# Kernel tuning notes

Hardware: AMD Instinct MI355X
Metric: run time of the kernel (lower is better)

The kernel has to match this reference:

```python
import jax, jax.numpy as jnp
import numpy as np

# static config matching init_kwargs
NODE, K, KER, STR = 32, 10, 5, 2
B, C = 8, 64
N = NODE * NODE          # 1024 nodes per sample
BN = B * N               # 8192 total nodes
OUT = (NODE - KER) // STR + 1
E = OUT * OUT            # local hyperedges per sample (196)
BN_EPS = 1e-5


def _local_block_diag():
    """Static block-diagonal local incidence matrix (BN, B*E), built once in numpy."""
    idx = np.arange(N).reshape(NODE, NODE)
    H_local = np.zeros((N, E), np.float32)
    e = 0
    for i in range(0, NODE - KER + 1, STR):
        for j in range(0, NODE - KER + 1, STR):
            H_local[idx[i:i + KER, j:j + KER].ravel(), e] = 1.0
            e += 1
    blk = np.zeros((BN, B * E), np.float32)
    for b in range(B):
        blk[b * N:(b + 1) * N, b * E:(b + 1) * E] = H_local
    return jnp.asarray(blk)


_LOCAL_BLK = _local_block_diag()


def setup_inputs() -> dict:
    key = jax.random.key(0)
    k1, k2 = jax.random.split(key, 2)
    x = jax.random.normal(k1, (B, N, C), jnp.float32)
    W_conv = jax.random.normal(k2, (C, C), jnp.float32) * 0.05
    b_conv = jnp.zeros((C,), jnp.float32)
    gamma = jnp.ones((C,), jnp.float32)
    beta = jnp.zeros((C,), jnp.float32)
    return {"x": x, "W_conv": W_conv, "b_conv": b_conv, "gamma": gamma, "beta": beta}


def reference(x, W_conv, b_conv, gamma, beta):
    xm = x.reshape(BN, C)                       # merged nodes (B*N, C)

    # --- hypergraph construction (no_grad in torch) ---
    xs = jax.lax.stop_gradient(xm)
    sq = jnp.sum(xs * xs, axis=-1, keepdims=True)
    dists = sq - 2.0 * (xs @ xs.T) + sq.T       # (BN, BN) pairwise sq-dists
    _, inds = jax.lax.top_k(-dists, K + 1)      # K+1 smallest distances
    # weights_function(prob=False) -> all ones; scatter incidence
    H = jnp.zeros((BN, BN), x.dtype).at[jnp.arange(BN)[:, None], inds].set(1.0)
    # Dv == K+1 for every row -> max_k = K+1 and the second topk gives new_H == H
    Hfull = jnp.concatenate([H, _LOCAL_BLK], axis=1)  # (BN, BN + B*E)

    # G = Dv^{-1/2} H W De^{-1} H^T Dv^{-1/2}, W = I, via diagonal scaling
    DV = Hfull.sum(axis=1)
    DE = jnp.maximum(Hfull.sum(axis=0), 1e-8)
    dv2 = DV ** -0.5
    A = dv2[:, None] * Hfull
    G = (A * (1.0 / DE)[None, :]) @ A.T          # (BN, BN)
    G = jax.lax.stop_gradient(G)

    # --- HGNN conv: linear -> G matmul -> BN (train stats) -> relu -> residual ---
    y = xm @ W_conv.T + b_conv                   # (BN, C)
    z = G @ y                                    # (BN, C)
    mu = z.mean(axis=0)
    var = z.var(axis=0)                          # biased, as torch BN training
    zn = (z - mu) / jnp.sqrt(var + BN_EPS) * gamma + beta
    out = jax.nn.relu(zn) + xm
    return out.reshape(B, N, C)
```

## Files before the change

kernel.cpp:

```cpp
#include <hip/hip_runtime.h>
#include <math.h>

#define BNTOT 8192
#define CH    64
#define KP1   11
#define NLOC  1568
#define CAP   256
#define LCAP  32
#define MARGIN 1.0f
#define DELTA  2.0f

typedef __attribute__((ext_vector_type(8))) short short8;
typedef __attribute__((ext_vector_type(4))) float float4v;

__device__ __forceinline__ int pcnt(int p) {
  int lo = p - 4; if (lo < 0) lo = 0; lo += (lo & 1);
  int hi = p; if (hi > 26) hi = 26;
  return (hi >= lo) ? (((hi - lo) >> 1) + 1) : 0;
}
__device__ __forceinline__ float dv2_of(int u) {
  int node = u & 1023;
  int rr = node >> 5, cc = node & 31;
  int dv = KP1 + pcnt(rr) * pcnt(cc);
  return 1.0f / sqrtf((float)dv);
}
__device__ __forceinline__ unsigned short f2bf(float f) {
  unsigned u = __float_as_uint(f);
  unsigned r = (u + 0x7FFFu + ((u >> 16) & 1u)) >> 16;
  return (unsigned short)r;
}
__device__ __forceinline__ unsigned long long skey(float s, int idx) {
  unsigned u = __float_as_uint(s);
  u = (u & 0x80000000u) ? ~u : (u | 0x80000000u);
  return ((unsigned long long)u << 32) | (unsigned)idx;
}

__global__ void k_cast(const float* __restrict__ X, unsigned short* __restrict__ Xh,
                       float* __restrict__ sq) {
  int g = blockIdx.x * 256 + threadIdx.x;
  int lane = threadIdx.x & 63;
  float v = X[g];
  Xh[g] = f2bf(v);
  float s = v * v;
  #pragma unroll
  for (int off = 32; off >= 1; off >>= 1) s += __shfl_xor(s, off, 64);
  if (lane == 0) sq[g >> 6] = s;
}

__global__ __launch_bounds__(256)
void k_thrpart(const float* __restrict__ X, const float* __restrict__ sq,
               float* __restrict__ part) {
  const int tid = threadIdx.x, wave = tid >> 6, lane = tid & 63;
  const int rg = blockIdx.x >> 3, chunk = blockIdx.x & 7;
  const int row = rg * 64 + lane;
  float xr[CH];
  {
    const float4* xp = (const float4*)(X + (size_t)row * CH);
    #pragma unroll
    for (int k = 0; k < CH / 4; ++k) {
      float4 v = xp[k];
      xr[4*k+0] = v.x; xr[4*k+1] = v.y; xr[4*k+2] = v.z; xr[4*k+3] = v.w;
    }
  }
  float tv[KP1];
  #pragma unroll
  for (int t = 0; t < KP1; ++t) tv[t] = INFINITY;

  for (int s = 0; s < 32; ++s) {
    int j = __builtin_amdgcn_readfirstlane(((chunk * 4 + wave) * 32 + s) * 8);
    const float* cp = X + (size_t)j * CH;
    float d0 = 0.f, d1 = 0.f, d2 = 0.f, d3 = 0.f;
    #pragma unroll
    for (int k = 0; k < CH / 4; ++k) {
      d0 = fmaf(xr[4*k+0], cp[4*k+0], d0);
      d1 = fmaf(xr[4*k+1], cp[4*k+1], d1);
      d2 = fmaf(xr[4*k+2], cp[4*k+2], d2);
      d3 = fmaf(xr[4*k+3], cp[4*k+3], d3);
    }
    float cv = fmaf(-2.0f, (d0 + d1) + (d2 + d3), sq[j]);
    #pragma unroll
    for (int t = 0; t < KP1; ++t) {
      float lo = fminf(tv[t], cv), hi = fmaxf(tv[t], cv);
      tv[t] = lo; cv = hi;
    }
  }
  __shared__ float ls[4][64][KP1];
  #pragma unroll
  for (int t = 0; t < KP1; ++t) ls[wave][lane][t] = tv[t];
  __syncthreads();
  if (tid < 64) {
    float v[KP1];
    #pragma unroll
    for (int t = 0; t < KP1; ++t) v[t] = ls[0][tid][t];
    #pragma unroll
    for (int w = 1; w < 4; ++w)
      #pragma unroll
      for (int t = 0; t < KP1; ++t) {
        float cv = ls[w][tid][t];
        #pragma unroll
        for (int s2 = 0; s2 < KP1; ++s2) {
          float lo = fminf(v[s2], cv), hi = fmaxf(v[s2], cv);
          v[s2] = lo; cv = hi;
        }
      }
    size_t base = ((size_t)blockIdx.x * 64 + tid) * KP1;
    #pragma unroll
    for (int t = 0; t < KP1; ++t) part[base + t] = v[t];
  }
}

__global__ void k_thrmerge(const float* __restrict__ part, float* __restrict__ thr) {
  const int rg = blockIdx.x, lane = threadIdx.x;
  const int row = rg * 64 + lane;
  float v[KP1];
  {
    size_t b0 = ((size_t)(rg * 8) * 64 + lane) * KP1;
    #pragma unroll
    for (int t = 0; t < KP1; ++t) v[t] = part[b0 + t];
  }
  for (int c = 1; c < 8; ++c) {
    size_t b = ((size_t)(rg * 8 + c) * 64 + lane) * KP1;
    #pragma unroll
    for (int t = 0; t < KP1; ++t) {
      float cv = part[b + t];
      #pragma unroll
      for (int s2 = 0; s2 < KP1; ++s2) {
        float lo = fminf(v[s2], cv), hi = fmaxf(v[s2], cv);
        v[s2] = lo; cv = hi;
      }
    }
  }
  thr[row] = v[KP1 - 1] + MARGIN;
}

__global__ __launch_bounds__(256)
void k_filter(const unsigned short* __restrict__ Xh, const float* __restrict__ sq,
              const float* __restrict__ thr, int* __restrict__ cnt,
              uint2* __restrict__ cand) {
  __shared__ uint2 lcand[64][LCAP];
  __shared__ int lcnt[64];
  __shared__ int lbase[64];

  const int tid = threadIdx.x, wave = tid >> 6, lane = tid & 63;
  const int m = lane & 15, q = lane >> 4;
  const int rowbase = (blockIdx.x >> 5) * 64;
  const int colbase = (blockIdx.x & 31) * 256 + wave * 64;

  if (tid < 64) lcnt[tid] = 0;

  short8 a[4][2];
  #pragma unroll
  for (int rt = 0; rt < 4; ++rt)
    #pragma unroll
    for (int kc = 0; kc < 2; ++kc)
      a[rt][kc] = *(const short8*)(Xh + (size_t)(rowbase + rt * 16 + m) * CH + kc * 32 + q * 8);

  short8 b0[4], b1[4];
  float sqv[4];
  #pragma unroll
  for (int sub = 0; sub < 4; ++sub) {
    const int coln = colbase + sub * 16 + m;
    const short8* bp = (const short8*)(Xh + (size_t)coln * CH + q * 8);
    b0[sub] = bp[0];
    b1[sub] = bp[4];
    sqv[sub] = sq[coln];
  }

  float thrv[16];
  #pragma unroll
  for (int rt = 0; rt < 4; ++rt)
    #pragma unroll
    for (int r = 0; r < 4; ++r)
      thrv[rt * 4 + r] = thr[rowbase + rt * 16 + q * 4 + r];

  __syncthreads();

  const float4v cz = {0.f, 0.f, 0.f, 0.f};
  #pragma unroll
  for (int sub = 0; sub < 4; ++sub) {
    const int coln = colbase + sub * 16 + m;
    #pragma unroll
    for (int rt = 0; rt < 4; ++rt) {
      float4v c = __builtin_amdgcn_mfma_f32_16x16x32_bf16(a[rt][0], b0[sub], cz, 0, 0, 0);
      c = __builtin_amdgcn_mfma_f32_16x16x32_bf16(a[rt][1], b1[sub], c, 0, 0, 0);
      #pragma unroll
      for (int r = 0; r < 4; ++r) {
        float score = fmaf(-2.0f, c[r], sqv[sub]);
        if (score < thrv[rt * 4 + r]) {
          int rl = rt * 16 + q * 4 + r;
          uint2 ent; ent.x = (unsigned)coln; ent.y = __float_as_uint(score);
          int s = atomicAdd(&lcnt[rl], 1);
          if (s < LCAP) {
            lcand[rl][s] = ent;
          } else {
            int gs = atomicAdd(&cnt[rowbase + rl], 1);
            if (gs < CAP) cand[(size_t)(rowbase + rl) * CAP + gs] = ent;
          }
        }
      }
    }
  }

  __syncthreads();
  if (tid < 64) {
    int nl = lcnt[tid]; if (nl > LCAP) nl = LCAP;
    lbase[tid] = atomicAdd(&cnt[rowbase + tid], nl);
    lcnt[tid] = nl;
  }
  __syncthreads();
  if (tid < 64) {
    int nl = lcnt[tid], base = lbase[tid];
    uint2* dst = cand + (size_t)(rowbase + tid) * CAP;
    for (int s = 0; s < nl; ++s) {
      int g = base + s;
      if (g < CAP) dst[g] = lcand[tid][s];
    }
  }
}

__global__ __launch_bounds__(256)
void k_rescore(const float* __restrict__ X, const float* __restrict__ sq,
               const int* __restrict__ cnt, const uint2* __restrict__ cand,
               int* __restrict__ inds, int* __restrict__ DE) {
  const int tid = threadIdx.x, lane = tid & 63;
  const int row = __builtin_amdgcn_readfirstlane(blockIdx.x * 4 + (tid >> 6));

  float xr[CH];
  {
    const float4* xp = (const float4*)(X + (size_t)row * CH);
    #pragma unroll
    for (int k = 0; k < CH / 4; ++k) {
      float4 v = xp[k];
      xr[4*k+0] = v.x; xr[4*k+1] = v.y; xr[4*k+2] = v.z; xr[4*k+3] = v.w;
    }
  }
  const int nraw = cnt[row];

  float tv[KP1]; int ti[KP1];
  #pragma unroll
  for (int t = 0; t < KP1; ++t) { tv[t] = INFINITY; ti[t] = -1; }

  if (nraw <= CAP) {
    const int n = nraw;
    const int slotcnt = (n + 63) >> 6;

    float bsc[4]; int bcol[4];
    #pragma unroll
    for (int a = 0; a < 4; ++a) { bsc[a] = INFINITY; bcol[a] = -1; }
    for (int a = 0; a < slotcnt; ++a) {
      int s = a * 64 + lane;
      if (s < n) {
        uint2 e = cand[(size_t)row * CAP + s];
        bcol[a] = (int)e.x; bsc[a] = __uint_as_float(e.y);
      }
    }
    float curf = bsc[0];
    #pragma unroll
    for (int a = 1; a < 4; ++a) curf = fminf(curf, bsc[a]);
    float c11 = INFINITY;
    #pragma unroll
    for (int t = 0; t < KP1; ++t) {
      float mw = curf;
      #pragma unroll
      for (int off = 1; off < 64; off <<= 1) mw = fminf(mw, __shfl_xor(mw, off, 64));
      if (t == KP1 - 1) c11 = mw;
      if (curf == mw) curf = INFINITY;
    }
    const float cutoff = c11 + DELTA;

    for (int a = 0; a < slotcnt; ++a) {
      if (bsc[a] <= cutoff) {
        int cj = bcol[a];
        const float4* cp = (const float4*)(X + (size_t)cj * CH);
        float d0 = 0.f, d1 = 0.f, d2 = 0.f, d3 = 0.f;
        #pragma unroll
        for (int k = 0; k < CH / 4; ++k) {
          float4 v = cp[k];
          d0 = fmaf(xr[4*k+0], v.x, d0);
          d1 = fmaf(xr[4*k+1], v.y, d1);
          d2 = fmaf(xr[4*k+2], v.z, d2);
          d3 = fmaf(xr[4*k+3], v.w, d3);
        }
        float score = fmaf(-2.0f, (d0 + d1) + (d2 + d3), sq[cj]);
        if (score < tv[KP1 - 1]) {
          float cv = score; int ci = cj;
          #pragma unroll
          for (int t = 0; t < KP1; ++t) {
            bool sw = cv < tv[t];
            float nv = sw ? cv   : tv[t]; int ni = sw ? ci   : ti[t];
            float ov = sw ? tv[t] : cv;   int oi = sw ? ti[t] : ci;
            tv[t] = nv; ti[t] = ni; cv = ov; ci = oi;
          }
        }
      }
    }
  } else {
    for (int s = lane; s < BNTOT; s += 64) {
      const float4* cp = (const float4*)(X + (size_t)s * CH);
      float d0 = 0.f, d1 = 0.f, d2 = 0.f, d3 = 0.f;
      #pragma unroll
      for (int k = 0; k < CH / 4; ++k) {
        float4 v = cp[k];
        d0 = fmaf(xr[4*k+0], v.x, d0);
        d1 = fmaf(xr[4*k+1], v.y, d1);
        d2 = fmaf(xr[4*k+2], v.z, d2);
        d3 = fmaf(xr[4*k+3], v.w, d3);
      }
      float score = fmaf(-2.0f, (d0 + d1) + (d2 + d3), sq[s]);
      if (score < tv[KP1 - 1]) {
        float cv = score; int ci = s;
        #pragma unroll
        for (int t = 0; t < KP1; ++t) {
          bool sw = cv < tv[t];
          float nv = sw ? cv   : tv[t]; int ni = sw ? ci   : ti[t];
          float ov = sw ? tv[t] : cv;   int oi = sw ? ti[t] : ci;
          tv[t] = nv; ti[t] = ni; cv = ov; ci = oi;
        }
      }
    }
  }

  unsigned long long cur = skey(tv[0], ti[0]);
  unsigned long long keep = 0;
  #pragma unroll
  for (int t = 0; t < KP1; ++t) {
    unsigned long long mw = cur;
    #pragma unroll
    for (int off = 1; off < 64; off <<= 1) {
      unsigned lo = __shfl_xor((unsigned)mw, off, 64);
      unsigned hi = __shfl_xor((unsigned)(mw >> 32), off, 64);
      unsigned long long o = ((unsigned long long)hi << 32) | lo;
      mw = (o < mw) ? o : mw;
    }
    if (lane == t) keep = mw;
    if (cur == mw) {
      #pragma unroll
      for (int q = 0; q < KP1 - 1; ++q) { tv[q] = tv[q+1]; ti[q] = ti[q+1]; }
      tv[KP1-1] = INFINITY; ti[KP1-1] = -1;
      cur = skey(tv[0], ti[0]);
    }
  }
  if (lane < KP1) {
    int idx = (int)(unsigned)(keep & 0xFFFFFFFFull);
    inds[(size_t)row * KP1 + lane] = idx;
    atomicAdd(&DE[idx], 1);
  }
}

__global__ void k_lin(const float* __restrict__ X, const float* __restrict__ W,
                      const float* __restrict__ bias, float* __restrict__ t) {
  int lane = threadIdx.x & 63;
  int wave = threadIdx.x >> 6;
  int rowbase = (blockIdx.x * 4 + wave) * 4;
  float wr[CH];
  {
    const float4* wp = (const float4*)(W + (size_t)lane * CH);
    #pragma unroll
    for (int k = 0; k < CH / 4; ++k) {
      float4 v = wp[k];
      wr[4*k+0] = v.x; wr[4*k+1] = v.y; wr[4*k+2] = v.z; wr[4*k+3] = v.w;
    }
  }
  float bc = bias[lane];
  #pragma unroll
  for (int r = 0; r < 4; ++r) {
    int row = __builtin_amdgcn_readfirstlane(rowbase + r);
    const float* xp = X + (size_t)row * CH;
    float d0 = 0.f, d1 = 0.f, d2 = 0.f, d3 = 0.f;
    #pragma unroll
    for (int k = 0; k < CH / 4; ++k) {
      d0 = fmaf(wr[4*k+0], xp[4*k+0], d0);
      d1 = fmaf(wr[4*k+1], xp[4*k+1], d1);
      d2 = fmaf(wr[4*k+2], xp[4*k+2], d2);
      d3 = fmaf(wr[4*k+3], xp[4*k+3], d3);
    }
    float y = (d0 + d1) + (d2 + d3) + bc;
    t[(size_t)row * CH + lane] = y * dv2_of(row);
  }
}

__global__ void k_edge(const float* __restrict__ t, const int* __restrict__ inds,
                       float* __restrict__ s_knn, float* __restrict__ s_loc) {
  int c = threadIdx.x & 63;
  int w = threadIdx.x >> 6;
  if (blockIdx.x < BNTOT / 4) {
    int u = blockIdx.x * 4 + w;
    float val = t[(size_t)u * CH + c];
    int ub = __builtin_amdgcn_readfirstlane(u);
    const int* ip = inds + (size_t)ub * KP1;
    #pragma unroll
    for (int j = 0; j < KP1; ++j) {
      int e = ip[j];
      atomicAdd(&s_knn[(size_t)e * CH + c], val);
    }
  } else {
    int e = (blockIdx.x - BNTOT / 4) * 4 + w;
    int b  = e / 196;
    int le = e - b * 196;
    int pi = le / 14;
    int pj = le - pi * 14;
    int base = b * 1024 + (pi * 2) * 32 + pj * 2;
    float acc = 0.f;
    #pragma unroll
    for (int di = 0; di < 5; ++di)
      #pragma unroll
      for (int dj = 0; dj < 5; ++dj)
        acc += t[(size_t)(base + di * 32 + dj) * CH + c];
    s_loc[(size_t)e * CH + c] = acc * (1.0f / 25.0f);
  }
}

__global__ void k_gatherbn(const float* __restrict__ s_knn, const float* __restrict__ s_loc,
                           const int* __restrict__ inds, const int* __restrict__ DE,
                           float* __restrict__ z, float* __restrict__ part,
                           float* __restrict__ partsq) {
  int c = threadIdx.x & 63;
  int w = threadIdx.x >> 6;
  int u = blockIdx.x * 4 + w;
  int ub = __builtin_amdgcn_readfirstlane(u);
  const int* ip = inds + (size_t)ub * KP1;
  float acc = 0.f;
  #pragma unroll
  for (int j = 0; j < KP1; ++j) {
    int e = ip[j];
    float invde = 1.0f / (float)DE[e];
    acc += s_knn[(size_t)e * CH + c] * invde;
  }
  int node = ub & 1023, b = ub >> 10;
  int rr = node >> 5, cc = node & 31;
  int i0 = rr - 4; if (i0 < 0) i0 = 0; i0 += (i0 & 1);
  int i1 = rr; if (i1 > 26) i1 = 26;
  int j0 = cc - 4; if (j0 < 0) j0 = 0; j0 += (j0 & 1);
  int j1 = cc; if (j1 > 26) j1 = 26;
  for (int i = i0; i <= i1; i += 2)
    for (int jj = j0; jj <= j1; jj += 2) {
      int e = b * 196 + (i >> 1) * 14 + (jj >> 1);
      acc += s_loc[(size_t)e * CH + c];
    }
  float zv = acc * dv2_of(ub);
  z[(size_t)ub * CH + c] = zv;

  __shared__ float ls[4][CH], ls2[4][CH];
  ls[w][c] = zv; ls2[w][c] = zv * zv;
  __syncthreads();
  if (threadIdx.x < 64) {
    part[(size_t)blockIdx.x * CH + c]   = ls[0][c] + ls[1][c] + ls[2][c] + ls[3][c];
    partsq[(size_t)blockIdx.x * CH + c] = ls2[0][c] + ls2[1][c] + ls2[2][c] + ls2[3][c];
  }
}

__global__ void k_bnfin1(const float* __restrict__ part, const float* __restrict__ partsq,
                         float* __restrict__ part2, float* __restrict__ partsq2) {
  int c = threadIdx.x & 63;
  int rq = threadIdx.x >> 6;
  int blk = blockIdx.x;
  float s = 0.f, s2 = 0.f;
  for (int k = 0; k < 16; ++k) {
    size_t r = (size_t)(blk * 64 + rq * 16 + k) * CH + c;
    s += part[r]; s2 += partsq[r];
  }
  __shared__ float ls[4][CH], ls2[4][CH];
  ls[rq][c] = s; ls2[rq][c] = s2;
  __syncthreads();
  if (rq == 0) {
    part2[(size_t)blk * CH + c]   = ls[0][c] + ls[1][c] + ls[2][c] + ls[3][c];
    partsq2[(size_t)blk * CH + c] = ls2[0][c] + ls2[1][c] + ls2[2][c] + ls2[3][c];
  }
}

__global__ void k_out(const float* __restrict__ z, const float* __restrict__ X,
                      const float* __restrict__ part2, const float* __restrict__ partsq2,
                      const float* __restrict__ gamma, const float* __restrict__ beta,
                      float* __restrict__ out) {
  __shared__ float ls[4][CH], ls2[4][CH], smu[CH], srstd[CH];
  int c = threadIdx.x & 63;
  int w = threadIdx.x >> 6;
  float s = 0.f, s2 = 0.f;
  #pragma unroll
  for (int b = 0; b < 8; ++b) {
    size_t r = (size_t)(w * 8 + b) * CH + c;
    s += part2[r]; s2 += partsq2[r];
  }
  ls[w][c] = s; ls2[w][c] = s2;
  __syncthreads();
  if (threadIdx.x < 64) {
    float S  = ls[0][c] + ls[1][c] + ls[2][c] + ls[3][c];
    float S2 = ls2[0][c] + ls2[1][c] + ls2[2][c] + ls2[3][c];
    float m = S * (1.0f / (float)BNTOT);
    float var = S2 * (1.0f / (float)BNTOT) - m * m;
    smu[c] = m;
    srstd[c] = 1.0f / sqrtf(var + 1e-5f);
  }
  __syncthreads();

  int u = blockIdx.x * 4 + w;
  size_t idx = (size_t)u * CH + c;
  float zn = (z[idx] - smu[c]) * srstd[c] * gamma[c] + beta[c];
  out[idx] = fmaxf(zn, 0.f) + X[idx];
}

extern "C" void kernel_launch(void* const* d_in, const int* in_sizes, int n_in,
                              void* d_out, int out_size, void* d_ws, size_t ws_size,
                              hipStream_t stream) {
  const float* X     = (const float*)d_in[0];
  const float* W     = (const float*)d_in[1];
  const float* bias  = (const float*)d_in[2];
  const float* gamma = (const float*)d_in[3];
  const float* beta  = (const float*)d_in[4];
  float* out = (float*)d_out;

  float* ws = (float*)d_ws;
  float* sq      = ws;
  float* thr     = sq + 8192;
  float* t       = thr + 8192;
  float* s_loc   = t + 524288;
  float* z       = s_loc + 100352;
  float* part    = z + 524288;
  float* partsq  = part + 131072;
  float* part2   = partsq + 131072;
  float* partsq2 = part2 + 2048;
  float* thrpart = partsq2 + 2048;
  int*   inds    = (int*)(thrpart + 720896);
  unsigned short* Xh = (unsigned short*)(inds + 90112);
  uint2* cand    = (uint2*)(Xh + 524288);
  int*   cnt    = (int*)(cand + (size_t)8192 * CAP);
  int*   DE     = cnt + 8192;
  float* s_knn  = (float*)(DE + 8192);

  hipMemsetAsync(cnt, 0, (size_t)(8192 + 8192 + 524288) * 4, stream);

  k_cast    <<<2048, 256, 0, stream>>>(X, Xh, sq);
  k_thrpart <<<1024, 256, 0, stream>>>(X, sq, thrpart);
  k_thrmerge<<<128, 64, 0, stream>>>(thrpart, thr);
  k_filter  <<<4096, 256, 0, stream>>>(Xh, sq, thr, cnt, cand);
  k_rescore <<<2048, 256, 0, stream>>>(X, sq, cnt, cand, inds, DE);
  k_lin     <<<512, 256, 0, stream>>>(X, W, bias, t);
  k_edge    <<<BNTOT / 4 + NLOC / 4, 256, 0, stream>>>(t, inds, s_knn, s_loc);
  k_gatherbn<<<BNTOT / 4, 256, 0, stream>>>(s_knn, s_loc, inds, DE, z, part, partsq);
  k_bnfin1  <<<32, 256, 0, stream>>>(part, partsq, part2, partsq2);
  k_out     <<<BNTOT / 4, 256, 0, stream>>>(z, X, part2, partsq2, gamma, beta, out);

  (void)in_sizes; (void)n_in; (void)out_size; (void)ws_size;
}
```

Baseline: 231.7 us.

## Replace atomic candidate lists with ballot-built bitmasks for kNN filtering

The filter kernel now records which columns pass the per-row threshold as a dense 8192-bit mask per row, built with wave ballots, in place of appending (column, score) pairs through shared and global atomics. The rescore kernel walks the set bits of its row's mask and recomputes exact fp32 distances for every candidate. This drops the atomics, shared staging, syncthreads and candidate-count memset, and removes the full-scan overflow fallback. In exchange the second-stage cutoff pruning (DELTA) is gone, so every thresholded candidate is rescored, and each lane's work depends on how many bits land in its 128-column slice, which can be uneven.

Result: slower. 243.5 us (+5.1%).

```diff
diff --git a/kernel.cpp b/kernel.cpp
--- a/kernel.cpp
+++ b/kernel.cpp
@@ -5,10 +5,7 @@
 #define CH    64
 #define KP1   11
 #define NLOC  1568
-#define CAP   256
-#define LCAP  32
 #define MARGIN 1.0f
-#define DELTA  2.0f
 
 typedef __attribute__((ext_vector_type(8))) short short8;
 typedef __attribute__((ext_vector_type(4))) float float4v;
@@ -135,18 +132,12 @@
 
 __global__ __launch_bounds__(256)
 void k_filter(const unsigned short* __restrict__ Xh, const float* __restrict__ sq,
-              const float* __restrict__ thr, int* __restrict__ cnt,
-              uint2* __restrict__ cand) {
-  __shared__ uint2 lcand[64][LCAP];
-  __shared__ int lcnt[64];
-  __shared__ int lbase[64];
-
+              const float* __restrict__ thr, unsigned long long* __restrict__ mask) {
   const int tid = threadIdx.x, wave = tid >> 6, lane = tid & 63;
   const int m = lane & 15, q = lane >> 4;
   const int rowbase = (blockIdx.x >> 5) * 64;
   const int colbase = (blockIdx.x & 31) * 256 + wave * 64;
-
-  if (tid < 64) lcnt[tid] = 0;
+  const int wcol = (blockIdx.x & 31) * 4 + wave;
 
   short8 a[4][2];
   #pragma unroll
@@ -173,54 +164,40 @@
     for (int r = 0; r < 4; ++r)
       thrv[rt * 4 + r] = thr[rowbase + rt * 16 + q * 4 + r];
 
-  __syncthreads();
-
   const float4v cz = {0.f, 0.f, 0.f, 0.f};
-  #pragma unroll
-  for (int sub = 0; sub < 4; ++sub) {
-    const int coln = colbase + sub * 16 + m;
-    #pragma unroll
-    for (int rt = 0; rt < 4; ++rt) {
+  const int sr = lane & 15, qq = sr >> 2, rr = sr & 3;
+
+  #pragma unroll
+  for (int rt = 0; rt < 4; ++rt) {
+    unsigned long long bal[4][4];
+    #pragma unroll
+    for (int sub = 0; sub < 4; ++sub) {
       float4v c = __builtin_amdgcn_mfma_f32_16x16x32_bf16(a[rt][0], b0[sub], cz, 0, 0, 0);
       c = __builtin_amdgcn_mfma_f32_16x16x32_bf16(a[rt][1], b1[sub], c, 0, 0, 0);
       #pragma unroll
       for (int r = 0; r < 4; ++r) {
         float score = fmaf(-2.0f, c[r], sqv[sub]);
-        if (score < thrv[rt * 4 + r]) {
-          int rl = rt * 16 + q * 4 + r;
-          uint2 ent; ent.x = (unsigned)coln; ent.y = __float_as_uint(score);
-          int s = atomicAdd(&lcnt[rl], 1);
-          if (s < LCAP) {
-            lcand[rl][s] = ent;
-          } else {
-            int gs = atomicAdd(&cnt[rowbase + rl], 1);
-            if (gs < CAP) cand[(size_t)(rowbase + rl) * CAP + gs] = ent;
-          }
-        }
+        bal[sub][r] = __ballot(score < thrv[rt * 4 + r]);
       }
     }
-  }
-
-  __syncthreads();
-  if (tid < 64) {
-    int nl = lcnt[tid]; if (nl > LCAP) nl = LCAP;
-    lbase[tid] = atomicAdd(&cnt[rowbase + tid], nl);
-    lcnt[tid] = nl;
-  }
-  __syncthreads();
-  if (tid < 64) {
-    int nl = lcnt[tid], base = lbase[tid];
-    uint2* dst = cand + (size_t)(rowbase + tid) * CAP;
-    for (int s = 0; s < nl; ++s) {
-      int g = base + s;
-      if (g < CAP) dst[g] = lcand[tid][s];
-    }
+    unsigned long long w = 0;
+    #pragma unroll
+    for (int sub = 0; sub < 4; ++sub) {
+      unsigned long long bsel = (rr == 0) ? bal[sub][0]
+                              : (rr == 1) ? bal[sub][1]
+                              : (rr == 2) ? bal[sub][2]
+                              :             bal[sub][3];
+      unsigned long long slice = (bsel >> (qq * 16)) & 0xFFFFull;
+      w |= slice << (sub * 16);
+    }
+    if ((lane >> 4) == rt)
+      mask[(size_t)(rowbase + rt * 16 + sr) * 128 + wcol] = w;
   }
 }
 
 __global__ __launch_bounds__(256)
 void k_rescore(const float* __restrict__ X, const float* __restrict__ sq,
-               const int* __restrict__ cnt, const uint2* __restrict__ cand,
+               const unsigned long long* __restrict__ mask,
                int* __restrict__ inds, int* __restrict__ DE) {
   const int tid = threadIdx.x, lane = tid & 63;
   const int row = __builtin_amdgcn_readfirstlane(blockIdx.x * 4 + (tid >> 6));
@@ -234,69 +211,24 @@
       xr[4*k+0] = v.x; xr[4*k+1] = v.y; xr[4*k+2] = v.z; xr[4*k+3] = v.w;
     }
   }
-  const int nraw = cnt[row];
 
   float tv[KP1]; int ti[KP1];
   #pragma unroll
   for (int t = 0; t < KP1; ++t) { tv[t] = INFINITY; ti[t] = -1; }
 
-  if (nraw <= CAP) {
-    const int n = nraw;
-    const int slotcnt = (n + 63) >> 6;
-
-    float bsc[4]; int bcol[4];
-    #pragma unroll
-    for (int a = 0; a < 4; ++a) { bsc[a] = INFINITY; bcol[a] = -1; }
-    for (int a = 0; a < slotcnt; ++a) {
-      int s = a * 64 + lane;
-      if (s < n) {
-        uint2 e = cand[(size_t)row * CAP + s];
-        bcol[a] = (int)e.x; bsc[a] = __uint_as_float(e.y);
-      }
-    }
-    float curf = bsc[0];
-    #pragma unroll
-    for (int a = 1; a < 4; ++a) curf = fminf(curf, bsc[a]);
-    float c11 = INFINITY;
-    #pragma unroll
-    for (int t = 0; t < KP1; ++t) {
-      float mw = curf;
-      #pragma unroll
-      for (int off = 1; off < 64; off <<= 1) mw = fminf(mw, __shfl_xor(mw, off, 64));
-      if (t == KP1 - 1) c11 = mw;
-      if (curf == mw) curf = INFINITY;
-    }
-    const float cutoff = c11 + DELTA;
-
-    for (int a = 0; a < slotcnt; ++a) {
-      if (bsc[a] <= cutoff) {
-        int cj = bcol[a];
-        const float4* cp = (const float4*)(X + (size_t)cj * CH);
-        float d0 = 0.f, d1 = 0.f, d2 = 0.f, d3 = 0.f;
-        #pragma unroll
-        for (int k = 0; k < CH / 4; ++k) {
-          float4 v = cp[k];
-          d0 = fmaf(xr[4*k+0], v.x, d0);
-          d1 = fmaf(xr[4*k+1], v.y, d1);
-          d2 = fmaf(xr[4*k+2], v.z, d2);
-          d3 = fmaf(xr[4*k+3], v.w, d3);
-        }
-        float score = fmaf(-2.0f, (d0 + d1) + (d2 + d3), sq[cj]);
-        if (score < tv[KP1 - 1]) {
-          float cv = score; int ci = cj;
-          #pragma unroll
-          for (int t = 0; t < KP1; ++t) {
-            bool sw = cv < tv[t];
-            float nv = sw ? cv   : tv[t]; int ni = sw ? ci   : ti[t];
-            float ov = sw ? tv[t] : cv;   int oi = sw ? ti[t] : ci;
-            tv[t] = nv; ti[t] = ni; cv = ov; ci = oi;
-          }
-        }
-      }
-    }
-  } else {
-    for (int s = lane; s < BNTOT; s += 64) {
-      const float4* cp = (const float4*)(X + (size_t)s * CH);
+  const unsigned long long* mrow = mask + (size_t)row * 128;
+  unsigned long long w0 = mrow[lane * 2 + 0];
+  unsigned long long w1 = mrow[lane * 2 + 1];
+
+  #pragma unroll
+  for (int h = 0; h < 2; ++h) {
+    unsigned long long w = h ? w1 : w0;
+    const int base = lane * 128 + h * 64;
+    while (w) {
+      int b = __builtin_ctzll(w);
+      w &= (w - 1);
+      int cj = base + b;
+      const float4* cp = (const float4*)(X + (size_t)cj * CH);
       float d0 = 0.f, d1 = 0.f, d2 = 0.f, d3 = 0.f;
       #pragma unroll
       for (int k = 0; k < CH / 4; ++k) {
@@ -306,13 +238,14 @@
         d2 = fmaf(xr[4*k+2], v.z, d2);
         d3 = fmaf(xr[4*k+3], v.w, d3);
       }
-      float score = fmaf(-2.0f, (d0 + d1) + (d2 + d3), sq[s]);
+      float score = fmaf(-2.0f, (d0 + d1) + (d2 + d3), sq[cj]);
       if (score < tv[KP1 - 1]) {
-        float cv = score; int ci = s;
+        float cv = score; int ci = cj;
         #pragma unroll
         for (int t = 0; t < KP1; ++t) {
           bool sw = cv < tv[t];
-          float nv = sw ? cv   : tv[t]; int ni = sw ? ci   : ti[t];
+          float nv = sw ? cv   : tv[t]; int ni = sw ? ti[t] : ti[t];
+          ni = sw ? ci : ti[t];
           float ov = sw ? tv[t] : cv;   int oi = sw ? ti[t] : ci;
           tv[t] = nv; ti[t] = ni; cv = ov; ci = oi;
         }
@@ -522,18 +455,17 @@
   float* thrpart = partsq2 + 2048;
   int*   inds    = (int*)(thrpart + 720896);
   unsigned short* Xh = (unsigned short*)(inds + 90112);
-  uint2* cand    = (uint2*)(Xh + 524288);
-  int*   cnt    = (int*)(cand + (size_t)8192 * CAP);
-  int*   DE     = cnt + 8192;
+  unsigned long long* mask = (unsigned long long*)(Xh + 524288);
+  int*   DE     = (int*)(mask + (size_t)8192 * 128);
   float* s_knn  = (float*)(DE + 8192);
 
-  hipMemsetAsync(cnt, 0, (size_t)(8192 + 8192 + 524288) * 4, stream);
+  hipMemsetAsync(DE, 0, (size_t)(8192 + 524288) * 4, stream);
 
   k_cast    <<<2048, 256, 0, stream>>>(X, Xh, sq);
   k_thrpart <<<1024, 256, 0, stream>>>(X, sq, thrpart);
   k_thrmerge<<<128, 64, 0, stream>>>(thrpart, thr);
-  k_filter  <<<4096, 256, 0, stream>>>(Xh, sq, thr, cnt, cand);
-  k_rescore <<<2048, 256, 0, stream>>>(X, sq, cnt, cand, inds, DE);
+  k_filter  <<<4096, 256, 0, stream>>>(Xh, sq, thr, mask);
+  k_rescore <<<2048, 256, 0, stream>>>(X, sq, mask, inds, DE);
   k_lin     <<<512, 256, 0, stream>>>(X, W, bias, t);
   k_edge    <<<BNTOT / 4 + NLOC / 4, 256, 0, stream>>>(t, inds, s_knn, s_loc);
   k_gatherbn<<<BNTOT / 4, 256, 0, stream>>>(s_knn, s_loc, inds, DE, z, part, partsq);
```
